# Kernel tuning notes

Measured on AMD Instinct MI355X. Metric: run time of the kernel, lower is better.

Reference implementation:

```python
import jax, jax.numpy as jnp
import numpy as np

D_MODEL = 1024
VOCAB = 50257
N_TOK = 2048
LABEL_SMOOTHING = 0.1
PAD_ID = 1


def setup_inputs() -> dict:
    key = jax.random.key(0)
    k1, k2, k3, k4 = jax.random.split(key, 4)
    x = jax.random.normal(k1, (N_TOK, D_MODEL), dtype=jnp.float32)
    W = jax.random.normal(k2, (VOCAB, D_MODEL), dtype=jnp.float32) * (1.0 / np.sqrt(D_MODEL))
    b = jax.random.normal(k3, (VOCAB,), dtype=jnp.float32) * 0.01
    labels = jax.random.randint(k4, (N_TOK,), 0, VOCAB, dtype=jnp.int64)
    return {"x": x, "W": W, "b": b, "labels": labels}


def reference(x, W, b, labels):
    N, V = x.shape[0], W.shape[0]
    confidence = 1.0 - LABEL_SMOOTHING
    smoothing_value = LABEL_SMOOTHING / (V - 2)

    # scores: [N, V]
    scores = jnp.einsum('nd,vd->nv', x, W) + b
    log_q = jax.nn.log_softmax(scores, axis=-1)

    # smoothed target distribution truth_p: [N, V]
    one_hot = jnp.full((V,), smoothing_value, dtype=scores.dtype).at[PAD_ID].set(0.0)
    truth_p = jnp.broadcast_to(one_hot, (N, V))
    truth_p = truth_p.at[jnp.arange(N), labels].set(confidence)
    truth_p = jnp.where((labels == PAD_ID)[:, None], 0.0, truth_p)

    # KLDivLoss(reduction='sum'): sum_t p * (log p - log q), with 0*log0 := 0
    kl = jnp.where(truth_p > 0, truth_p * (jnp.log(jnp.where(truth_p > 0, truth_p, 1.0)) - log_q), 0.0)
    loss = kl.sum() / N
    return scores, loss
```

## Files before the change

### kernel.cpp

```cpp
#include <hip/hip_runtime.h>
#include <hip/hip_bf16.h>
#include <math.h>

#define D_MODEL 1024
#define VOCAB   50257
#define VPAD    50304
#define N_TOK   2048
#define PAD_ID  1

typedef __attribute__((ext_vector_type(8))) short bf16x8;
typedef __attribute__((ext_vector_type(4))) float f32x4;
typedef __attribute__((ext_vector_type(2))) unsigned int u32x2;
typedef __attribute__((ext_vector_type(4))) unsigned short u16x4;

static __device__ __forceinline__ unsigned int pack2bf(float a, float b) {
  unsigned int ua = (__float_as_uint(a) + 0x8000u) >> 16;
  unsigned int ub = (__float_as_uint(b) + 0x8000u) & 0xffff0000u;
  return ua | ub;
}
static __device__ __forceinline__ unsigned short bf16of(float a) {
  return (unsigned short)((__float_as_uint(a) + 0x8000u) >> 16);
}

static __device__ __forceinline__ void gload_lds16(const void* g, void* l) {
  __builtin_amdgcn_global_load_lds(
      (const __attribute__((address_space(1))) void*)g,
      (__attribute__((address_space(3))) void*)l, 16, 0, 0);
}

__global__ __launch_bounds__(256)
void cvt_f32_bf16(const float* __restrict__ in, unsigned short* __restrict__ out, int n4) {
  for (int i = blockIdx.x * blockDim.x + threadIdx.x; i < n4; i += gridDim.x * blockDim.x) {
    f32x4 v = *(const f32x4*)(in + 4 * (size_t)i);
    u16x4 o;
    o[0] = bf16of(v[0]); o[1] = bf16of(v[1]); o[2] = bf16of(v[2]); o[3] = bf16of(v[3]);
    *(u16x4*)(out + 4 * (size_t)i) = o;
  }
}

__global__ __launch_bounds__(256)
void zero_pad_rows(unsigned short* __restrict__ out, int n4) {
  int i = blockIdx.x * blockDim.x + threadIdx.x;
  if (i < n4) {
    u16x4 z = {0, 0, 0, 0};
    *(u16x4*)(out + 4 * (size_t)i) = z;
  }
}

__global__ __launch_bounds__(256)
void gemm_scores_bf16(const unsigned short* __restrict__ Xb, const unsigned short* __restrict__ Wb,
                      const float* __restrict__ bias, float* __restrict__ OUT)
{
  const int tid  = threadIdx.x;
  const int lane = tid & 63;
  const int wave = tid >> 6;
  const int m0 = blockIdx.y * 128;
  const int n0 = blockIdx.x * 128;
  const int wm = (wave >> 1) * 64;
  const int wn = (wave & 1) * 64;

  __shared__ __attribute__((aligned(16))) unsigned short As[128 * 32];
  __shared__ __attribute__((aligned(16))) unsigned short Bs[128 * 32];

  f32x4 acc[4][4] = {};

  const int frow = lane & 15;
  const int fk   = (lane >> 4) * 8;

  const int srow = (lane >> 2);
  const int scol = (lane & 3) * 8;

  for (int kt = 0; kt < D_MODEL / 32; ++kt) {
    const int k0 = kt * 32;

    __syncthreads();

#pragma unroll
    for (int i = 0; i < 2; ++i) {
      const int r = wave * 32 + i * 16;
      gload_lds16(Xb + (size_t)(m0 + r + srow) * D_MODEL + k0 + scol, &As[r * 32]);
      gload_lds16(Wb + (size_t)(n0 + r + srow) * D_MODEL + k0 + scol, &Bs[r * 32]);
    }

    __syncthreads();

    bf16x8 afrag[4], bfrag[4];
#pragma unroll
    for (int i = 0; i < 4; ++i)
      afrag[i] = *(const bf16x8*)&As[(wm + i * 16 + frow) * 32 + fk];
#pragma unroll
    for (int j = 0; j < 4; ++j)
      bfrag[j] = *(const bf16x8*)&Bs[(wn + j * 16 + frow) * 32 + fk];

#pragma unroll
    for (int i = 0; i < 4; ++i)
#pragma unroll
      for (int j = 0; j < 4; ++j)
        acc[i][j] = __builtin_amdgcn_mfma_f32_16x16x32_bf16(afrag[i], bfrag[j], acc[i][j], 0, 0, 0);
  }

  const int r4 = (lane >> 4) << 2;
  const int cc = lane & 15;
#pragma unroll
  for (int j = 0; j < 4; ++j) {
    const int col = n0 + wn + j * 16 + cc;
    if (col < VOCAB) {
      const float bj = bias[col];
#pragma unroll
      for (int i = 0; i < 4; ++i) {
        const int row = m0 + wm + i * 16 + r4;
        float* o = OUT + (size_t)row * VOCAB + col;
#pragma unroll
        for (int r = 0; r < 4; ++r)
          o[(size_t)r * VOCAB] = acc[i][j][r] + bj;
      }
    }
  }
}

__global__ __launch_bounds__(256)
void gemm_scores(const float* __restrict__ X, const float* __restrict__ W,
                 const float* __restrict__ bias, float* __restrict__ OUT)
{
  const int tid  = threadIdx.x;
  const int lane = tid & 63;
  const int wave = tid >> 6;
  const int m0 = blockIdx.y * 128;
  const int n0 = blockIdx.x * 128;
  const int wm = (wave >> 1) * 64;
  const int wn = (wave & 1) * 64;

  __shared__ __attribute__((aligned(16))) unsigned short As[128 * 32];
  __shared__ __attribute__((aligned(16))) unsigned short Bs[128 * 32];

  f32x4 acc[4][4] = {};

  const int frow = lane & 15;
  const int fk   = (lane >> 4) * 8;

  for (int kt = 0; kt < D_MODEL / 32; ++kt) {
    const int k0 = kt * 32;
    f32x4 av[4], bv[4];
#pragma unroll
    for (int i = 0; i < 4; ++i) {
      const int idx = tid + (i << 8);
      const int r = idx >> 3;
      const int c = (idx & 7) << 2;
      av[i] = *(const f32x4*)(X + (size_t)(m0 + r) * D_MODEL + k0 + c);
      int wr = n0 + r; if (wr > VOCAB - 1) wr = VOCAB - 1;
      bv[i] = *(const f32x4*)(W + (size_t)wr * D_MODEL + k0 + c);
    }
    __syncthreads();
#pragma unroll
    for (int i = 0; i < 4; ++i) {
      const int idx = tid + (i << 8);
      const int r = idx >> 3;
      const int c = (idx & 7) << 2;
      u32x2 pa, pb;
      pa[0] = pack2bf(av[i][0], av[i][1]);
      pa[1] = pack2bf(av[i][2], av[i][3]);
      pb[0] = pack2bf(bv[i][0], bv[i][1]);
      pb[1] = pack2bf(bv[i][2], bv[i][3]);
      *(u32x2*)&As[r * 32 + c] = pa;
      *(u32x2*)&Bs[r * 32 + c] = pb;
    }
    __syncthreads();

    bf16x8 afrag[4], bfrag[4];
#pragma unroll
    for (int i = 0; i < 4; ++i)
      afrag[i] = *(const bf16x8*)&As[(wm + i * 16 + frow) * 32 + fk];
#pragma unroll
    for (int j = 0; j < 4; ++j)
      bfrag[j] = *(const bf16x8*)&Bs[(wn + j * 16 + frow) * 32 + fk];
#pragma unroll
    for (int i = 0; i < 4; ++i)
#pragma unroll
      for (int j = 0; j < 4; ++j)
        acc[i][j] = __builtin_amdgcn_mfma_f32_16x16x32_bf16(afrag[i], bfrag[j], acc[i][j], 0, 0, 0);
  }

  const int r4 = (lane >> 4) << 2;
  const int cc = lane & 15;
#pragma unroll
  for (int j = 0; j < 4; ++j) {
    const int col = n0 + wn + j * 16 + cc;
    if (col < VOCAB) {
      const float bj = bias[col];
#pragma unroll
      for (int i = 0; i < 4; ++i) {
        const int row = m0 + wm + i * 16 + r4;
        float* o = OUT + (size_t)row * VOCAB + col;
#pragma unroll
        for (int r = 0; r < 4; ++r)
          o[(size_t)r * VOCAB] = acc[i][j][r] + bj;
      }
    }
  }
}

__global__ __launch_bounds__(256)
void row_stats_loss(const float* __restrict__ S, const int* __restrict__ labels,
                    float* __restrict__ loss)
{
  const int row = blockIdx.x;
  const int tid = threadIdx.x;
  const float* p = S + (size_t)row * VOCAB;

  float m = -INFINITY, s = 0.f, tot = 0.f;

  const int head = (4 - (row & 3)) & 3;
  if (tid < head) {
    float x = p[tid];
    tot = x; m = x; s = 1.f;
  }
  const int nvec = (VOCAB - head) >> 2;
  const float* pv = p + head;
  for (int i = tid; i < nvec; i += 256) {
    f32x4 x4 = *(const f32x4*)(pv + 4 * i);
#pragma unroll
    for (int e = 0; e < 4; ++e) {
      float x = x4[e];
      tot += x;
      float nm = fmaxf(m, x);
      if (nm > m) { s *= __expf(m - nm); m = nm; }
      s += __expf(x - m);
    }
  }
  const int tbase = head + 4 * nvec;
  if (tid < VOCAB - tbase) {
    float x = p[tbase + tid];
    tot += x;
    float nm = fmaxf(m, x);
    if (nm > m) { s *= __expf(m - nm); m = nm; }
    s += __expf(x - m);
  }

#pragma unroll
  for (int off = 1; off < 64; off <<= 1) {
    float om = __shfl_xor(m, off);
    float os = __shfl_xor(s, off);
    tot += __shfl_xor(tot, off);
    float nm = fmaxf(m, om);
    s = s * __expf(m - nm) + os * __expf(om - nm);
    m = nm;
  }

  __shared__ float red[12];
  const int wave = tid >> 6;
  if ((tid & 63) == 0) { red[wave] = m; red[4 + wave] = s; red[8 + wave] = tot; }
  __syncthreads();

  if (tid == 0) {
    m = red[0]; s = red[4]; tot = red[8];
    for (int w = 1; w < 4; ++w) {
      float om = red[w], os = red[4 + w];
      float nm = fmaxf(m, om);
      s = s * __expf(m - nm) + os * __expf(om - nm);
      m = nm;
      tot += red[8 + w];
    }
    const int lbl = labels[row];
    if (lbl != PAD_ID) {
      const float x_lbl = p[lbl];
      const float x_pad = p[PAD_ID];
      const float logZ = m + logf(s);
      const float sv   = 0.1f / (float)(VOCAB - 2);
      const float conf = 0.9f;
      const float plogp = 0.1f * logf(sv) + conf * logf(conf);
      const float plogq = sv * (tot - x_pad - x_lbl) + conf * x_lbl - logZ;
      atomicAdd(loss, (plogp - plogq) * (1.0f / N_TOK));
    }
  }
}

__global__ void zero_loss(float* loss) { *loss = 0.f; }

extern "C" void kernel_launch(void* const* d_in, const int* in_sizes, int n_in,
                              void* d_out, int out_size, void* d_ws, size_t ws_size,
                              hipStream_t stream) {
  const float* X      = (const float*)d_in[0];
  const float* W      = (const float*)d_in[1];
  const float* bias   = (const float*)d_in[2];
  const int*   labels = (const int*)d_in[3];
  float* out  = (float*)d_out;
  float* loss = out + (size_t)N_TOK * VOCAB;

  zero_loss<<<1, 1, 0, stream>>>(loss);

  const size_t wb_elems = (size_t)VPAD * D_MODEL;
  const size_t xb_elems = (size_t)N_TOK * D_MODEL;
  const size_t need = (wb_elems + xb_elems) * sizeof(unsigned short);

  dim3 grid(VPAD / 128, N_TOK / 128);

  if (ws_size >= need) {
    unsigned short* Wb = (unsigned short*)d_ws;
    unsigned short* Xb = Wb + wb_elems;
    cvt_f32_bf16<<<2048, 256, 0, stream>>>(W, Wb, (int)((size_t)VOCAB * D_MODEL / 4));
    {
      const int padn4 = (int)(((size_t)(VPAD - VOCAB) * D_MODEL) / 4);
      zero_pad_rows<<<(padn4 + 255) / 256, 256, 0, stream>>>(Wb + (size_t)VOCAB * D_MODEL, padn4);
    }
    cvt_f32_bf16<<<512, 256, 0, stream>>>(X, Xb, (int)(xb_elems / 4));
    gemm_scores_bf16<<<grid, 256, 0, stream>>>(Xb, Wb, bias, out);
  } else {
    gemm_scores<<<grid, 256, 0, stream>>>(X, W, bias, out);
  }

  row_stats_loss<<<N_TOK, 256, 0, stream>>>(out, labels, loss);
}
```

Measured before the change: 973.4 us.

## Fuse per-tile softmax statistics into GEMM epilogue and add XCD-aware tile swizzle

The GEMM epilogue now computes per-row partial max, sum-of-exp and total over each 128-column tile and writes them to a small workspace buffer. A light finalize kernel then merges these partials per row, so the separate pass that re-reads the full 2048x50257 score matrix is no longer needed. Block indices are also remapped so consecutive blocks across the 8 XCDs share W tiles, which should improve L2 reuse. The cost is extra epilogue shuffles and exps in the GEMM, plus a workspace requirement that falls back to the old two-pass path when the workspace is too small.

```diff
diff --git a/kernel.cpp b/kernel.cpp
--- a/kernel.cpp
+++ b/kernel.cpp
@@ -7,6 +7,10 @@
 #define VPAD    50304
 #define N_TOK   2048
 #define PAD_ID  1
+#define NTILE   (VPAD / 128)
+#define MTILE   (N_TOK / 128)
+#define NWG     (NTILE * MTILE)
+#define CPX     (NWG / 8)
 
 typedef __attribute__((ext_vector_type(8))) short bf16x8;
 typedef __attribute__((ext_vector_type(4))) float f32x4;
@@ -48,14 +52,188 @@
 }
 
 __global__ __launch_bounds__(256)
+void gemm_scores_fused(const unsigned short* __restrict__ Xb, const unsigned short* __restrict__ Wb,
+                       const float* __restrict__ bias, float* __restrict__ OUT,
+                       f32x4* __restrict__ partial)
+{
+  const int tid  = threadIdx.x;
+  const int lane = tid & 63;
+  const int wave = tid >> 6;
+
+  const int bid = blockIdx.x;
+  const int sw  = (bid & 7) * CPX + (bid >> 3);
+  const int m0     = (sw & 15) * 128;
+  const int n_tile = sw >> 4;
+  const int n0     = n_tile * 128;
+
+  const int wm = (wave >> 1) * 64;
+  const int wn = (wave & 1) * 64;
+
+  __shared__ __attribute__((aligned(16))) unsigned short As[128 * 32];
+  __shared__ __attribute__((aligned(16))) unsigned short Bs[128 * 32];
+  __shared__ f32x4 sred[128][2];
+
+  f32x4 acc[4][4] = {};
+
+  const int frow = lane & 15;
+  const int fk   = (lane >> 4) * 8;
+  const int srow = (lane >> 2);
+  const int scol = (lane & 3) * 8;
+
+  for (int kt = 0; kt < D_MODEL / 32; ++kt) {
+    const int k0 = kt * 32;
+
+    __syncthreads();
+
+#pragma unroll
+    for (int i = 0; i < 2; ++i) {
+      const int r = wave * 32 + i * 16;
+      gload_lds16(Xb + (size_t)(m0 + r + srow) * D_MODEL + k0 + scol, &As[r * 32]);
+      gload_lds16(Wb + (size_t)(n0 + r + srow) * D_MODEL + k0 + scol, &Bs[r * 32]);
+    }
+
+    __syncthreads();
+
+    bf16x8 afrag[4], bfrag[4];
+#pragma unroll
+    for (int i = 0; i < 4; ++i)
+      afrag[i] = *(const bf16x8*)&As[(wm + i * 16 + frow) * 32 + fk];
+#pragma unroll
+    for (int j = 0; j < 4; ++j)
+      bfrag[j] = *(const bf16x8*)&Bs[(wn + j * 16 + frow) * 32 + fk];
+
+#pragma unroll
+    for (int i = 0; i < 4; ++i)
+#pragma unroll
+      for (int j = 0; j < 4; ++j)
+        acc[i][j] = __builtin_amdgcn_mfma_f32_16x16x32_bf16(afrag[i], bfrag[j], acc[i][j], 0, 0, 0);
+  }
+
+  const int r4 = (lane >> 4) << 2;
+  const int cc = lane & 15;
+
+  float bj[4];
+  bool  vld[4];
+#pragma unroll
+  for (int j = 0; j < 4; ++j) {
+    const int col = n0 + wn + j * 16 + cc;
+    vld[j] = (col < VOCAB);
+    bj[j] = vld[j] ? bias[col] : 0.f;
+  }
+
+#pragma unroll
+  for (int i = 0; i < 4; ++i) {
+    const int rowl = wm + i * 16 + r4;
+#pragma unroll
+    for (int r = 0; r < 4; ++r) {
+      float v[4];
+#pragma unroll
+      for (int j = 0; j < 4; ++j) v[j] = acc[i][j][r] + bj[j];
+
+      float* orow = OUT + (size_t)(m0 + rowl + r) * VOCAB;
+#pragma unroll
+      for (int j = 0; j < 4; ++j)
+        if (vld[j]) orow[n0 + wn + j * 16 + cc] = v[j];
+
+      float tm = -INFINITY, tt = 0.f;
+#pragma unroll
+      for (int j = 0; j < 4; ++j) {
+        tm = fmaxf(tm, vld[j] ? v[j] : -INFINITY);
+        tt += vld[j] ? v[j] : 0.f;
+      }
+      float te = 0.f;
+#pragma unroll
+      for (int j = 0; j < 4; ++j)
+        te += vld[j] ? __expf(v[j] - tm) : 0.f;
+
+#pragma unroll
+      for (int off = 1; off < 16; off <<= 1) {
+        float om = __shfl_xor(tm, off);
+        float os = __shfl_xor(te, off);
+        float ot = __shfl_xor(tt, off);
+        float nm = fmaxf(tm, om);
+        te = te * __expf(tm - nm) + os * __expf(om - nm);
+        tm = nm;
+        tt += ot;
+      }
+      if (cc == 0) {
+        f32x4 p; p[0] = tm; p[1] = te; p[2] = tt; p[3] = 0.f;
+        sred[rowl + r][wave & 1] = p;
+      }
+    }
+  }
+
+  __syncthreads();
+  if (tid < 128) {
+    f32x4 a = sred[tid][0], b = sred[tid][1];
+    float nm = fmaxf(a[0], b[0]);
+    f32x4 p;
+    p[0] = nm;
+    p[1] = a[1] * __expf(a[0] - nm) + b[1] * __expf(b[0] - nm);
+    p[2] = a[2] + b[2];
+    p[3] = 0.f;
+    partial[(size_t)(m0 + tid) * NTILE + n_tile] = p;
+  }
+}
+
+__global__ __launch_bounds__(128)
+void finalize_loss(const f32x4* __restrict__ partial, const float* __restrict__ S,
+                   const int* __restrict__ labels, float* __restrict__ loss)
+{
+  const int row = blockIdx.x;
+  const int tid = threadIdx.x;
+
+  float m = -INFINITY, s = 0.f, t = 0.f;
+  for (int nt = tid; nt < NTILE; nt += 128) {
+    f32x4 p = partial[(size_t)row * NTILE + nt];
+    float nm = fmaxf(m, p[0]);
+    s = s * __expf(m - nm) + p[1] * __expf(p[0] - nm);
+    m = nm;
+    t += p[2];
+  }
+#pragma unroll
+  for (int off = 1; off < 64; off <<= 1) {
+    float om = __shfl_xor(m, off);
+    float os = __shfl_xor(s, off);
+    t += __shfl_xor(t, off);
+    float nm = fmaxf(m, om);
+    s = s * __expf(m - nm) + os * __expf(om - nm);
+    m = nm;
+  }
+  __shared__ float red[6];
+  if ((tid & 63) == 0) { int w = tid >> 6; red[w * 3] = m; red[w * 3 + 1] = s; red[w * 3 + 2] = t; }
+  __syncthreads();
+  if (tid == 0) {
+    float m2 = red[3], s2 = red[4];
+    float nm = fmaxf(red[0], m2);
+    float S_ = red[1] * __expf(red[0] - nm) + s2 * __expf(m2 - nm);
+    float T_ = red[2] + red[5];
+    const int lbl = labels[row];
+    if (lbl != PAD_ID) {
+      const float* p = S + (size_t)row * VOCAB;
+      const float x_lbl = p[lbl];
+      const float x_pad = p[PAD_ID];
+      const float logZ = nm + logf(S_);
+      const float sv   = 0.1f / (float)(VOCAB - 2);
+      const float conf = 0.9f;
+      const float plogp = 0.1f * logf(sv) + conf * logf(conf);
+      const float plogq = sv * (T_ - x_pad - x_lbl) + conf * x_lbl - logZ;
+      atomicAdd(loss, (plogp - plogq) * (1.0f / N_TOK));
+    }
+  }
+}
+
+__global__ __launch_bounds__(256)
 void gemm_scores_bf16(const unsigned short* __restrict__ Xb, const unsigned short* __restrict__ Wb,
                       const float* __restrict__ bias, float* __restrict__ OUT)
 {
   const int tid  = threadIdx.x;
   const int lane = tid & 63;
   const int wave = tid >> 6;
-  const int m0 = blockIdx.y * 128;
-  const int n0 = blockIdx.x * 128;
+  const int bid = blockIdx.x;
+  const int sw  = (bid & 7) * CPX + (bid >> 3);
+  const int m0 = (sw & 15) * 128;
+  const int n0 = (sw >> 4) * 128;
   const int wm = (wave >> 1) * 64;
   const int wn = (wave & 1) * 64;
 
@@ -63,25 +241,20 @@
   __shared__ __attribute__((aligned(16))) unsigned short Bs[128 * 32];
 
   f32x4 acc[4][4] = {};
-
   const int frow = lane & 15;
   const int fk   = (lane >> 4) * 8;
-
   const int srow = (lane >> 2);
   const int scol = (lane & 3) * 8;
 
   for (int kt = 0; kt < D_MODEL / 32; ++kt) {
     const int k0 = kt * 32;
-
-    __syncthreads();
-
+    __syncthreads();
 #pragma unroll
     for (int i = 0; i < 2; ++i) {
       const int r = wave * 32 + i * 16;
       gload_lds16(Xb + (size_t)(m0 + r + srow) * D_MODEL + k0 + scol, &As[r * 32]);
       gload_lds16(Wb + (size_t)(n0 + r + srow) * D_MODEL + k0 + scol, &Bs[r * 32]);
     }
-
     __syncthreads();
 
     bf16x8 afrag[4], bfrag[4];
@@ -91,7 +264,6 @@
 #pragma unroll
     for (int j = 0; j < 4; ++j)
       bfrag[j] = *(const bf16x8*)&Bs[(wn + j * 16 + frow) * 32 + fk];
-
 #pragma unroll
     for (int i = 0; i < 4; ++i)
 #pragma unroll
@@ -134,7 +306,6 @@
   __shared__ __attribute__((aligned(16))) unsigned short Bs[128 * 32];
 
   f32x4 acc[4][4] = {};
-
   const int frow = lane & 15;
   const int fk   = (lane >> 4) * 8;
 
@@ -208,12 +379,8 @@
   const float* p = S + (size_t)row * VOCAB;
 
   float m = -INFINITY, s = 0.f, tot = 0.f;
-
   const int head = (4 - (row & 3)) & 3;
-  if (tid < head) {
-    float x = p[tid];
-    tot = x; m = x; s = 1.f;
-  }
+  if (tid < head) { float x = p[tid]; tot = x; m = x; s = 1.f; }
   const int nvec = (VOCAB - head) >> 2;
   const float* pv = p + head;
   for (int i = tid; i < nvec; i += 256) {
@@ -235,7 +402,6 @@
     if (nm > m) { s *= __expf(m - nm); m = nm; }
     s += __expf(x - m);
   }
-
 #pragma unroll
   for (int off = 1; off < 64; off <<= 1) {
     float om = __shfl_xor(m, off);
@@ -245,12 +411,10 @@
     s = s * __expf(m - nm) + os * __expf(om - nm);
     m = nm;
   }
-
   __shared__ float red[12];
   const int wave = tid >> 6;
   if ((tid & 63) == 0) { red[wave] = m; red[4 + wave] = s; red[8 + wave] = tot; }
   __syncthreads();
-
   if (tid == 0) {
     m = red[0]; s = red[4]; tot = red[8];
     for (int w = 1; w < 4; ++w) {
@@ -290,11 +454,11 @@
 
   const size_t wb_elems = (size_t)VPAD * D_MODEL;
   const size_t xb_elems = (size_t)N_TOK * D_MODEL;
-  const size_t need = (wb_elems + xb_elems) * sizeof(unsigned short);
-
-  dim3 grid(VPAD / 128, N_TOK / 128);
-
-  if (ws_size >= need) {
+  const size_t need_gemm = (wb_elems + xb_elems) * sizeof(unsigned short);
+  const size_t part_bytes = (size_t)N_TOK * NTILE * sizeof(f32x4);
+  const size_t need_fused = need_gemm + part_bytes;
+
+  if (ws_size >= need_gemm) {
     unsigned short* Wb = (unsigned short*)d_ws;
     unsigned short* Xb = Wb + wb_elems;
     cvt_f32_bf16<<<2048, 256, 0, stream>>>(W, Wb, (int)((size_t)VOCAB * D_MODEL / 4));
@@ -303,10 +467,18 @@
       zero_pad_rows<<<(padn4 + 255) / 256, 256, 0, stream>>>(Wb + (size_t)VOCAB * D_MODEL, padn4);
     }
     cvt_f32_bf16<<<512, 256, 0, stream>>>(X, Xb, (int)(xb_elems / 4));
-    gemm_scores_bf16<<<grid, 256, 0, stream>>>(Xb, Wb, bias, out);
+
+    if (ws_size >= need_fused) {
+      f32x4* partial = (f32x4*)(Xb + xb_elems);
+      gemm_scores_fused<<<NWG, 256, 0, stream>>>(Xb, Wb, bias, out, partial);
+      finalize_loss<<<N_TOK, 128, 0, stream>>>(partial, out, labels, loss);
+    } else {
+      gemm_scores_bf16<<<NWG, 256, 0, stream>>>(Xb, Wb, bias, out);
+      row_stats_loss<<<N_TOK, 256, 0, stream>>>(out, labels, loss);
+    }
   } else {
+    dim3 grid(VPAD / 128, N_TOK / 128);
     gemm_scores<<<grid, 256, 0, stream>>>(X, W, bias, out);
-  }
-
-  row_stats_loss<<<N_TOK, 256, 0, stream>>>(out, labels, loss);
-}
+    row_stats_loss<<<N_TOK, 256, 0, stream>>>(out, labels, loss);
+  }
+}
```

Result: faster. 931.8 us (-4.3%).
